# Kernel optimization log

Measured on AMD Instinct MI355X. Metric: run time of the kernel, lower is better.

Reference implementation:

```python
import jax, jax.numpy as jnp
import numpy as np

DEGREE = 3
NUM_KNOTS = 256
T = 262144
S = 512
K = NUM_KNOTS + DEGREE - 1  # 258 basis functions


def bspline_basis(t, knots, degree):
    """Bottom-up (vectorized) Cox-de Boor recurrence.

    t: (T,), knots: (M,) with M = NUM_KNOTS + 2*degree.
    Returns basis matrix of shape (T, M - degree - 1).
    Matches the torch reference: degree-0 uses half-open interval
    [knots[i], knots[i+1]) and zero-denominator terms are dropped.
    """
    tc = t[:, None]  # (T, 1)
    # degree 0: (T, M-1)
    B = ((knots[None, :-1] <= tc) & (tc < knots[None, 1:])).astype(t.dtype)
    for d in range(1, degree + 1):
        n = B.shape[1] - 1  # number of basis funcs at degree d: M - d - 1
        k_i = knots[:n]             # knots[i]
        k_id = knots[d:d + n]       # knots[i+d]
        k_id1 = knots[d + 1:d + 1 + n]  # knots[i+d+1]
        k_i1 = knots[1:1 + n]       # knots[i+1]
        ld = k_id - k_i
        rd = k_id1 - k_i1
        left = jnp.where(ld != 0,
                         (tc - k_i) / jnp.where(ld != 0, ld, 1.0) * B[:, :n],
                         0.0)
        right = jnp.where(rd != 0,
                          (k_id1 - tc) / jnp.where(rd != 0, rd, 1.0) * B[:, 1:n + 1],
                          0.0)
        B = left + right
    return B  # (T, M - degree - 1)


def setup_inputs() -> dict:
    key = jax.random.key(0)
    k1, k2 = jax.random.split(key)
    times = jnp.sort(jax.random.uniform(k1, (T,), dtype=jnp.float32))
    # clamped knot vector, as in generate_knot_vector
    interior = jnp.linspace(times[0], times[-1], NUM_KNOTS)
    knots = jnp.concatenate([
        jnp.full((DEGREE,), times[0], dtype=jnp.float32),
        interior.astype(jnp.float32),
        jnp.full((DEGREE,), times[-1], dtype=jnp.float32),
    ])  # (NUM_KNOTS + 2*DEGREE,)
    weights = jax.random.normal(k2, (K, S), dtype=jnp.float32)
    return {"times": times, "weights": weights, "knots": knots}


def reference(times, weights, knots):
    B = bspline_basis(times, knots, DEGREE)       # (T, K)
    b_splines = B @ weights                        # (T, S)
    b_splines_sum = jnp.sum(b_splines, axis=1)     # (T,)
    return (b_splines, b_splines_sum)
```

## Files before the change

kernel.cpp:

```cpp
#include <hip/hip_runtime.h>

namespace {
constexpr int T_N = 262144;
constexpr int S_N = 512;
constexpr int K_N = 258;
constexpr int NK  = 262;
constexpr int ROWS_PER_WAVE = 32;
}

__global__ void wsum_kernel(const float* __restrict__ W, float* __restrict__ wsum) {
    const int row  = blockIdx.x * 4 + (threadIdx.x >> 6);
    const int lane = threadIdx.x & 63;
    if (row >= K_N) return;
    const float* wr = W + (size_t)row * S_N;
    float s = 0.f;
#pragma unroll
    for (int c = 0; c < S_N / 64; ++c) s += wr[lane + c * 64];
#pragma unroll
    for (int off = 32; off > 0; off >>= 1) s += __shfl_xor(s, off, 64);
    if (lane == 0) wsum[row] = s;
}

__global__ __launch_bounds__(256) void bspline_kernel(
    const float* __restrict__ times,
    const float* __restrict__ W,
    const float* __restrict__ knots,
    const float* __restrict__ wsum,
    float* __restrict__ out,
    float* __restrict__ out_sum)
{
    __shared__ float sk[NK];
    for (int i = threadIdx.x; i < NK; i += 256) sk[i] = knots[i];
    __syncthreads();

    const float k3    = sk[3];
    const float kend  = sk[NK - 4];
    const float inv_h = 255.0f / (kend - k3);

    const int wave = (int)((blockIdx.x * 256u + threadIdx.x) >> 6);
    const int lane = threadIdx.x & 63;
    const int row0 = wave * ROWS_PER_WAVE;

    const int colA = lane * 4;
    const int colB = colA + 256;

    int span = -1;
    float4 wA0, wA1, wA2, wA3, wB0, wB1, wB2, wB3;
    float ws0 = 0.f, ws1 = 0.f, ws2 = 0.f, ws3 = 0.f;

    for (int r = 0; r < ROWS_PER_WAVE; ++r) {
        const int row = row0 + r;
        const float t = times[row];
        float* op = out + (size_t)row * S_N;

        if (t >= kend) {
            const float4 z = make_float4(0.f, 0.f, 0.f, 0.f);
            *(float4*)(op + colA) = z;
            *(float4*)(op + colB) = z;
            if (lane == 0) out_sum[row] = 0.f;
            continue;
        }

        int i = 3 + (int)((t - k3) * inv_h);
        i = i < 3 ? 3 : (i > 257 ? 257 : i);
        while (t <  sk[i])     --i;
        while (t >= sk[i + 1]) ++i;

        float N0, N1, N2, N3;
        {
            const float left1  = t - sk[i];
            const float right1 = sk[i + 1] - t;
            const float left2  = t - sk[i - 1];
            const float right2 = sk[i + 2] - t;
            const float left3  = t - sk[i - 2];
            const float right3 = sk[i + 3] - t;
            float temp, saved;
            temp = 1.0f / (right1 + left1);
            N0 = right1 * temp;
            N1 = left1 * temp;
            temp = N0 / (right1 + left2);
            N0 = right1 * temp;
            saved = left2 * temp;
            temp = N1 / (right2 + left1);
            N1 = saved + right2 * temp;
            N2 = left1 * temp;
            temp = N0 / (right1 + left3);
            N0 = right1 * temp;
            saved = left3 * temp;
            temp = N1 / (right2 + left2);
            N1 = saved + right2 * temp;
            saved = left2 * temp;
            temp = N2 / (right3 + left1);
            N2 = saved + right3 * temp;
            N3 = left1 * temp;
        }

        if (i != span) {
            span = i;
            const float* wp = W + (size_t)(i - 3) * S_N;
            wA0 = *(const float4*)(wp + colA);
            wB0 = *(const float4*)(wp + colB);
            wA1 = *(const float4*)(wp + S_N + colA);
            wB1 = *(const float4*)(wp + S_N + colB);
            wA2 = *(const float4*)(wp + 2 * S_N + colA);
            wB2 = *(const float4*)(wp + 2 * S_N + colB);
            wA3 = *(const float4*)(wp + 3 * S_N + colA);
            wB3 = *(const float4*)(wp + 3 * S_N + colB);
            ws0 = wsum[i - 3]; ws1 = wsum[i - 2]; ws2 = wsum[i - 1]; ws3 = wsum[i];
        }

        float4 oa, ob;
        oa.x = N0 * wA0.x + N1 * wA1.x + N2 * wA2.x + N3 * wA3.x;
        oa.y = N0 * wA0.y + N1 * wA1.y + N2 * wA2.y + N3 * wA3.y;
        oa.z = N0 * wA0.z + N1 * wA1.z + N2 * wA2.z + N3 * wA3.z;
        oa.w = N0 * wA0.w + N1 * wA1.w + N2 * wA2.w + N3 * wA3.w;
        ob.x = N0 * wB0.x + N1 * wB1.x + N2 * wB2.x + N3 * wB3.x;
        ob.y = N0 * wB0.y + N1 * wB1.y + N2 * wB2.y + N3 * wB3.y;
        ob.z = N0 * wB0.z + N1 * wB1.z + N2 * wB2.z + N3 * wB3.z;
        ob.w = N0 * wB0.w + N1 * wB1.w + N2 * wB2.w + N3 * wB3.w;

        *(float4*)(op + colA) = oa;
        *(float4*)(op + colB) = ob;
        if (lane == 0)
            out_sum[row] = N0 * ws0 + N1 * ws1 + N2 * ws2 + N3 * ws3;
    }
}

extern "C" void kernel_launch(void* const* d_in, const int* in_sizes, int n_in,
                              void* d_out, int out_size, void* d_ws, size_t ws_size,
                              hipStream_t stream) {
    const float* times = (const float*)d_in[0];
    const float* W     = (const float*)d_in[1];
    const float* knots = (const float*)d_in[2];
    float* out     = (float*)d_out;
    float* out_sum = out + (size_t)T_N * S_N;
    float* wsum    = (float*)d_ws;

    wsum_kernel<<<(K_N + 3) / 4, 256, 0, stream>>>(W, wsum);

    const int nwaves = T_N / ROWS_PER_WAVE;
    bspline_kernel<<<nwaves / 4, 256, 0, stream>>>(times, W, knots, wsum, out, out_sum);
}
```

Measured before the change: 551.6 us.

## Compute basis per lane in parallel, stage in LDS, then stream rows

Each lane now computes the span and the four basis values for one row, instead of every lane redundantly computing them row by row. The results go into shared memory, and the wave then loops over its 64 rows writing outputs. A wave-uniform fast path loads the weights once when all rows share a span. The row sum is written per lane from an LDS copy of wsum. The change removes redundant scalar work and serial times loads from the store loop, at the cost of more LDS and fewer, longer-running waves.

Result: slower. 598.5 us (+8.5%).

```diff
diff --git a/kernel.cpp b/kernel.cpp
--- a/kernel.cpp
+++ b/kernel.cpp
@@ -5,7 +5,7 @@
 constexpr int S_N = 512;
 constexpr int K_N = 258;
 constexpr int NK  = 262;
-constexpr int ROWS_PER_WAVE = 32;
+constexpr int ROWS = 64;
 }
 
 __global__ void wsum_kernel(const float* __restrict__ W, float* __restrict__ wsum) {
@@ -29,100 +29,135 @@
     float* __restrict__ out,
     float* __restrict__ out_sum)
 {
-    __shared__ float sk[NK];
-    for (int i = threadIdx.x; i < NK; i += 256) sk[i] = knots[i];
+    __shared__ float  sk[NK];
+    __shared__ float  sws[K_N];
+    __shared__ float4 snf[4][ROWS];
+    __shared__ int    ssp[4][ROWS];
+
+    for (int idx = threadIdx.x; idx < NK;  idx += 256) sk[idx]  = knots[idx];
+    for (int idx = threadIdx.x; idx < K_N; idx += 256) sws[idx] = wsum[idx];
     __syncthreads();
+
+    const int wid  = threadIdx.x >> 6;
+    const int lane = threadIdx.x & 63;
+    const int row0 = (blockIdx.x * 4 + wid) * ROWS;
 
     const float k3    = sk[3];
     const float kend  = sk[NK - 4];
     const float inv_h = 255.0f / (kend - k3);
 
-    const int wave = (int)((blockIdx.x * 256u + threadIdx.x) >> 6);
-    const int lane = threadIdx.x & 63;
-    const int row0 = wave * ROWS_PER_WAVE;
+    const int myrow = row0 + lane;
+    const float t = times[myrow];
 
-    const int colA = lane * 4;
-    const int colB = colA + 256;
-
-    int span = -1;
-    float4 wA0, wA1, wA2, wA3, wB0, wB1, wB2, wB3;
-    float ws0 = 0.f, ws1 = 0.f, ws2 = 0.f, ws3 = 0.f;
-
-    for (int r = 0; r < ROWS_PER_WAVE; ++r) {
-        const int row = row0 + r;
-        const float t = times[row];
-        float* op = out + (size_t)row * S_N;
-
-        if (t >= kend) {
-            const float4 z = make_float4(0.f, 0.f, 0.f, 0.f);
-            *(float4*)(op + colA) = z;
-            *(float4*)(op + colB) = z;
-            if (lane == 0) out_sum[row] = 0.f;
-            continue;
-        }
-
-        int i = 3 + (int)((t - k3) * inv_h);
+    int i;
+    float N0, N1, N2, N3;
+    if (t >= kend) {
+        i = 257;
+        N0 = N1 = N2 = N3 = 0.f;
+    } else {
+        i = 3 + (int)((t - k3) * inv_h);
         i = i < 3 ? 3 : (i > 257 ? 257 : i);
         while (t <  sk[i])     --i;
         while (t >= sk[i + 1]) ++i;
 
-        float N0, N1, N2, N3;
-        {
-            const float left1  = t - sk[i];
-            const float right1 = sk[i + 1] - t;
-            const float left2  = t - sk[i - 1];
-            const float right2 = sk[i + 2] - t;
-            const float left3  = t - sk[i - 2];
-            const float right3 = sk[i + 3] - t;
-            float temp, saved;
-            temp = 1.0f / (right1 + left1);
-            N0 = right1 * temp;
-            N1 = left1 * temp;
-            temp = N0 / (right1 + left2);
-            N0 = right1 * temp;
-            saved = left2 * temp;
-            temp = N1 / (right2 + left1);
-            N1 = saved + right2 * temp;
-            N2 = left1 * temp;
-            temp = N0 / (right1 + left3);
-            N0 = right1 * temp;
-            saved = left3 * temp;
-            temp = N1 / (right2 + left2);
-            N1 = saved + right2 * temp;
-            saved = left2 * temp;
-            temp = N2 / (right3 + left1);
-            N2 = saved + right3 * temp;
-            N3 = left1 * temp;
+        const float left1  = t - sk[i];
+        const float right1 = sk[i + 1] - t;
+        const float left2  = t - sk[i - 1];
+        const float right2 = sk[i + 2] - t;
+        const float left3  = t - sk[i - 2];
+        const float right3 = sk[i + 3] - t;
+        float temp, saved;
+        temp = 1.0f / (right1 + left1);
+        N0 = right1 * temp;
+        N1 = left1 * temp;
+        temp = N0 / (right1 + left2);
+        N0 = right1 * temp;
+        saved = left2 * temp;
+        temp = N1 / (right2 + left1);
+        N1 = saved + right2 * temp;
+        N2 = left1 * temp;
+        temp = N0 / (right1 + left3);
+        N0 = right1 * temp;
+        saved = left3 * temp;
+        temp = N1 / (right2 + left2);
+        N1 = saved + right2 * temp;
+        saved = left2 * temp;
+        temp = N2 / (right3 + left1);
+        N2 = saved + right3 * temp;
+        N3 = left1 * temp;
+    }
+
+    out_sum[myrow] = N0 * sws[i - 3] + N1 * sws[i - 2] + N2 * sws[i - 1] + N3 * sws[i];
+
+    snf[wid][lane] = make_float4(N0, N1, N2, N3);
+    ssp[wid][lane] = i;
+
+    const int colA = lane * 4;
+    const int colB = colA + 256;
+    float* op0 = out + (size_t)row0 * S_N;
+
+    const int  i0  = __builtin_amdgcn_readfirstlane(i);
+    const bool uni = __all(i == i0);
+
+    if (uni) {
+        const float* wp = W + (size_t)(i0 - 3) * S_N;
+        const float4 wA0 = *(const float4*)(wp + colA);
+        const float4 wB0 = *(const float4*)(wp + colB);
+        const float4 wA1 = *(const float4*)(wp + S_N + colA);
+        const float4 wB1 = *(const float4*)(wp + S_N + colB);
+        const float4 wA2 = *(const float4*)(wp + 2 * S_N + colA);
+        const float4 wB2 = *(const float4*)(wp + 2 * S_N + colB);
+        const float4 wA3 = *(const float4*)(wp + 3 * S_N + colA);
+        const float4 wB3 = *(const float4*)(wp + 3 * S_N + colB);
+
+#pragma unroll 4
+        for (int r = 0; r < ROWS; ++r) {
+            const float4 n = snf[wid][r];
+            float* op = op0 + (size_t)r * S_N;
+            float4 oa, ob;
+            oa.x = n.x * wA0.x + n.y * wA1.x + n.z * wA2.x + n.w * wA3.x;
+            oa.y = n.x * wA0.y + n.y * wA1.y + n.z * wA2.y + n.w * wA3.y;
+            oa.z = n.x * wA0.z + n.y * wA1.z + n.z * wA2.z + n.w * wA3.z;
+            oa.w = n.x * wA0.w + n.y * wA1.w + n.z * wA2.w + n.w * wA3.w;
+            ob.x = n.x * wB0.x + n.y * wB1.x + n.z * wB2.x + n.w * wB3.x;
+            ob.y = n.x * wB0.y + n.y * wB1.y + n.z * wB2.y + n.w * wB3.y;
+            ob.z = n.x * wB0.z + n.y * wB1.z + n.z * wB2.z + n.w * wB3.z;
+            ob.w = n.x * wB0.w + n.y * wB1.w + n.z * wB2.w + n.w * wB3.w;
+            *(float4*)(op + colA) = oa;
+            *(float4*)(op + colB) = ob;
         }
-
-        if (i != span) {
-            span = i;
-            const float* wp = W + (size_t)(i - 3) * S_N;
-            wA0 = *(const float4*)(wp + colA);
-            wB0 = *(const float4*)(wp + colB);
-            wA1 = *(const float4*)(wp + S_N + colA);
-            wB1 = *(const float4*)(wp + S_N + colB);
-            wA2 = *(const float4*)(wp + 2 * S_N + colA);
-            wB2 = *(const float4*)(wp + 2 * S_N + colB);
-            wA3 = *(const float4*)(wp + 3 * S_N + colA);
-            wB3 = *(const float4*)(wp + 3 * S_N + colB);
-            ws0 = wsum[i - 3]; ws1 = wsum[i - 2]; ws2 = wsum[i - 1]; ws3 = wsum[i];
+    } else {
+        int span = -1;
+        float4 wA0 = make_float4(0,0,0,0), wA1 = wA0, wA2 = wA0, wA3 = wA0;
+        float4 wB0 = wA0, wB1 = wA0, wB2 = wA0, wB3 = wA0;
+        for (int r = 0; r < ROWS; ++r) {
+            const int ir = ssp[wid][r];
+            if (ir != span) {
+                span = ir;
+                const float* wp = W + (size_t)(ir - 3) * S_N;
+                wA0 = *(const float4*)(wp + colA);
+                wB0 = *(const float4*)(wp + colB);
+                wA1 = *(const float4*)(wp + S_N + colA);
+                wB1 = *(const float4*)(wp + S_N + colB);
+                wA2 = *(const float4*)(wp + 2 * S_N + colA);
+                wB2 = *(const float4*)(wp + 2 * S_N + colB);
+                wA3 = *(const float4*)(wp + 3 * S_N + colA);
+                wB3 = *(const float4*)(wp + 3 * S_N + colB);
+            }
+            const float4 n = snf[wid][r];
+            float* op = op0 + (size_t)r * S_N;
+            float4 oa, ob;
+            oa.x = n.x * wA0.x + n.y * wA1.x + n.z * wA2.x + n.w * wA3.x;
+            oa.y = n.x * wA0.y + n.y * wA1.y + n.z * wA2.y + n.w * wA3.y;
+            oa.z = n.x * wA0.z + n.y * wA1.z + n.z * wA2.z + n.w * wA3.z;
+            oa.w = n.x * wA0.w + n.y * wA1.w + n.z * wA2.w + n.w * wA3.w;
+            ob.x = n.x * wB0.x + n.y * wB1.x + n.z * wB2.x + n.w * wB3.x;
+            ob.y = n.x * wB0.y + n.y * wB1.y + n.z * wB2.y + n.w * wB3.y;
+            ob.z = n.x * wB0.z + n.y * wB1.z + n.z * wB2.z + n.w * wB3.z;
+            ob.w = n.x * wB0.w + n.y * wB1.w + n.z * wB2.w + n.w * wB3.w;
+            *(float4*)(op + colA) = oa;
+            *(float4*)(op + colB) = ob;
         }
-
-        float4 oa, ob;
-        oa.x = N0 * wA0.x + N1 * wA1.x + N2 * wA2.x + N3 * wA3.x;
-        oa.y = N0 * wA0.y + N1 * wA1.y + N2 * wA2.y + N3 * wA3.y;
-        oa.z = N0 * wA0.z + N1 * wA1.z + N2 * wA2.z + N3 * wA3.z;
-        oa.w = N0 * wA0.w + N1 * wA1.w + N2 * wA2.w + N3 * wA3.w;
-        ob.x = N0 * wB0.x + N1 * wB1.x + N2 * wB2.x + N3 * wB3.x;
-        ob.y = N0 * wB0.y + N1 * wB1.y + N2 * wB2.y + N3 * wB3.y;
-        ob.z = N0 * wB0.z + N1 * wB1.z + N2 * wB2.z + N3 * wB3.z;
-        ob.w = N0 * wB0.w + N1 * wB1.w + N2 * wB2.w + N3 * wB3.w;
-
-        *(float4*)(op + colA) = oa;
-        *(float4*)(op + colB) = ob;
-        if (lane == 0)
-            out_sum[row] = N0 * ws0 + N1 * ws1 + N2 * ws2 + N3 * ws3;
     }
 }
 
@@ -138,6 +173,6 @@
 
     wsum_kernel<<<(K_N + 3) / 4, 256, 0, stream>>>(W, wsum);
 
-    const int nwaves = T_N / ROWS_PER_WAVE;
-    bspline_kernel<<<nwaves / 4, 256, 0, stream>>>(times, W, knots, wsum, out, out_sum);
+    const int nblocks = T_N / (4 * ROWS);
+    bspline_kernel<<<nblocks, 256, 0, stream>>>(times, W, knots, wsum, out, out_sum);
 }
```
